# Performance work log

Hardware: AMD Instinct MI355X
Metric: run time of the kernel (lower is better)

## Reference

```python
import jax, jax.numpy as jnp
import numpy as np

B, L, D = 2, 2048, 2048
NUM_HEADS, NUM_KV_HEADS, HEAD_DIM = 8, 4, 256
GROUPS = NUM_HEADS // NUM_KV_HEADS
ROPE_BASE, ROPE_SCALE, ROPE_PROP = 10000.0, 1.0, 1.0
WINDOW = 1024
SOFT_CAP = 50.0
K_MASK = -2.3819763e+38
EPS = 1e-6


def rms_norm(x, scale):
    # RMSNorm(head_dim, with_scale=True, scale_plus_one=False), fp32 internals
    xf = x.astype(jnp.float32)
    var = jnp.mean(jnp.square(xf), axis=-1, keepdims=True)
    return (xf * jax.lax.rsqrt(var + EPS) * scale).astype(x.dtype)


def apply_rope(x, positions):
    # x: [B, L, N, H]; Gemma-style half-split rotation over rope_proportion of H
    H = x.shape[-1]
    rope_dim = int(H * ROPE_PROP)
    half = rope_dim // 2
    freq = ROPE_BASE ** (2.0 * jnp.arange(half, dtype=jnp.float32) / rope_dim)
    t = positions.astype(jnp.float32)[:, :, None] / freq[None, None, :]  # [B,L,half]
    t = t / ROPE_SCALE
    sin = jnp.sin(t)[:, :, None, :]  # [B,L,1,half]
    cos = jnp.cos(t)[:, :, None, :]
    x1 = x[..., :half]
    x2 = x[..., half:rope_dim]
    rotated = jnp.concatenate([x1 * cos - x2 * sin, x2 * cos + x1 * sin], axis=-1)
    if rope_dim < H:
        rotated = jnp.concatenate([rotated, x[..., rope_dim:]], axis=-1)
    return rotated.astype(x.dtype)


def setup_inputs() -> dict:
    key = jax.random.key(0)
    ks = jax.random.split(key, 8)
    x = jax.random.normal(ks[0], (B, L, D), dtype=jnp.float32)
    positions = jnp.broadcast_to(jnp.arange(L, dtype=jnp.int32)[None, :], (B, L))
    attn_mask = jnp.broadcast_to(jnp.tril(jnp.ones((L, L), dtype=bool))[None], (B, L, L))
    s = 0.02
    wq = jax.random.normal(ks[1], (D, NUM_HEADS * HEAD_DIM), dtype=jnp.float32) * s
    wk = jax.random.normal(ks[2], (D, NUM_KV_HEADS * HEAD_DIM), dtype=jnp.float32) * s
    wv = jax.random.normal(ks[3], (D, NUM_KV_HEADS * HEAD_DIM), dtype=jnp.float32) * s
    wo = jax.random.normal(ks[4], (NUM_HEADS * HEAD_DIM, D), dtype=jnp.float32) * s
    q_scale = 1.0 + 0.02 * jax.random.normal(ks[5], (HEAD_DIM,), dtype=jnp.float32)
    k_scale = 1.0 + 0.02 * jax.random.normal(ks[6], (HEAD_DIM,), dtype=jnp.float32)
    return {"x": x, "positions": positions, "attn_mask": attn_mask,
            "wq": wq, "wk": wk, "wv": wv, "wo": wo,
            "q_scale": q_scale, "k_scale": k_scale}


def reference(x, positions, attn_mask, wq, wk, wv, wo, q_scale, k_scale):
    q = (x @ wq).reshape(B, L, NUM_HEADS, HEAD_DIM)
    k = (x @ wk).reshape(B, L, NUM_KV_HEADS, HEAD_DIM)
    v = (x @ wv).reshape(B, L, NUM_KV_HEADS, HEAD_DIM)
    q = rms_norm(q, q_scale)
    k = rms_norm(k, k_scale)
    q = apply_rope(q, positions)
    k = apply_rope(k, positions)
    # query_pre_attn_scalar == 1.0 in source (no-op)
    qg = q.reshape(B, L, NUM_KV_HEADS, GROUPS, HEAD_DIM)
    logits = jnp.einsum('blkgh,bskh->blkgs', qg, k).reshape(B, L, NUM_HEADS, L)
    logits = jnp.tanh(logits / SOFT_CAP) * SOFT_CAP
    # sliding-window mask (LOCAL_SLIDING, no cache -> cache_positions = positions)
    cp = positions[:, None, :]
    pp = positions[:, :, None]
    slide = (cp > pp - WINDOW) & (cp < pp + WINDOW)
    mask = attn_mask & slide  # [B, L, S]
    padded = jnp.where(mask[:, :, None, :], logits, K_MASK)
    probs = jax.nn.softmax(padded, axis=-1).astype(k.dtype)
    pg = probs.reshape(B, L, NUM_KV_HEADS, GROUPS, L)
    out = jnp.einsum('blkgs,bskh->blkgh', pg, v).reshape(B, L, NUM_HEADS * HEAD_DIM)
    return out @ wo
```

## Files before the change

kernel.cpp:

```cpp
#include <hip/hip_runtime.h>
#include <stdint.h>

typedef unsigned short u16;
typedef __bf16 bf16x8 __attribute__((ext_vector_type(8)));
typedef float f32x4 __attribute__((ext_vector_type(4)));

#define SEQ 2048
#define NH 8
#define NKVH 4
#define HD 256
#define WIN 1024
#define NBATCH 2

__device__ __forceinline__ u16 f2bf(float f) {
    union { float f; unsigned u; } v; v.f = f;
    unsigned r = v.u + 0x7FFFu + ((v.u >> 16) & 1u);
    return (u16)(r >> 16);
}
__device__ __forceinline__ float bf2f(u16 h) {
    union { unsigned u; float f; } v; v.u = ((unsigned)h) << 16;
    return v.f;
}
__device__ __forceinline__ bf16x8 ld8(const u16* p) {
    return *reinterpret_cast<const bf16x8*>(p);
}
__device__ __forceinline__ void split2(float f, u16& h, u16& l) {
    h = f2bf(f);
    l = f2bf(f - bf2f(h));
}
__device__ __forceinline__ void gld16(const u16* gp, u16* lp) {
    __builtin_amdgcn_global_load_lds(
        (__attribute__((address_space(1))) unsigned int*)gp,
        (__attribute__((address_space(3))) unsigned int*)lp, 16, 0, 0);
}
#define MFMA16(a, b, c) __builtin_amdgcn_mfma_f32_16x16x32_bf16((a), (b), (c), 0, 0, 0)

__global__ void k_cvt_x(const float* __restrict__ in, u16* __restrict__ hi,
                        u16* __restrict__ lo, int n) {
    int i = (blockIdx.x * blockDim.x + threadIdx.x) * 4;
    if (i >= n) return;
    float4 v = *reinterpret_cast<const float4*>(in + i);
    ushort4 oh, ol;
    split2(v.x, oh.x, ol.x); split2(v.y, oh.y, ol.y);
    split2(v.z, oh.z, ol.z); split2(v.w, oh.w, ol.w);
    *reinterpret_cast<ushort4*>(hi + i) = oh;
    *reinterpret_cast<ushort4*>(lo + i) = ol;
}

__global__ void k_wt(const float* __restrict__ src, u16* __restrict__ dh,
                     u16* __restrict__ dl, int ncols) {
    __shared__ float tile[64][65];
    int c0 = blockIdx.x * 64;
    int k0 = blockIdx.y * 64;
    int tx = threadIdx.x & 63, ty = threadIdx.x >> 6;
    #pragma unroll
    for (int r = 0; r < 16; ++r) {
        int k = k0 + ty * 16 + r;
        tile[ty * 16 + r][tx] = src[(size_t)k * ncols + c0 + tx];
    }
    __syncthreads();
    #pragma unroll
    for (int r = 0; r < 16; ++r) {
        int c = c0 + ty * 16 + r;
        float f = tile[tx][ty * 16 + r];
        u16 h, l; split2(f, h, l);
        dh[(size_t)c * 2048 + k0 + tx] = h;
        dl[(size_t)c * 2048 + k0 + tx] = l;
    }
}

__global__ __launch_bounds__(256, 4) void k_gemm(
        const u16* __restrict__ A0, const u16* __restrict__ B0,
        const u16* __restrict__ A1, const u16* __restrict__ B1,
        const u16* __restrict__ A2, const u16* __restrict__ B2,
        float* __restrict__ C, int M, int N, int K, int nseg, int vcol0) {
    __shared__ __align__(16) u16 sA[128 * 64];
    __shared__ __align__(16) u16 sB[128 * 64];
    const int tm = blockIdx.x * 128;
    const int tn = blockIdx.y * 128;
    const int tid = threadIdx.x;
    const int lane = tid & 63;
    const int wave = tid >> 6;
    const int wr = (wave >> 1) * 64;
    const int wc = (wave & 1) * 64;
    const int l16 = lane & 15;
    const int g = lane >> 4;
    const int srow = tid >> 3;
    const int schunk = tid & 7;
    const int nseg_eff = (tn >= vcol0) ? 1 : nseg;
    f32x4 acc[4][4] = {};

    for (int seg = 0; seg < nseg_eff; ++seg) {
        const u16* A = seg == 0 ? A0 : (seg == 1 ? A1 : A2);
        const u16* B = seg == 0 ? B0 : (seg == 1 ? B1 : B2);
        for (int k0 = 0; k0 < K; k0 += 64) {
            __syncthreads();
            #pragma unroll
            for (int i = 0; i < 4; ++i) {
                int row = i * 32 + srow;
                int cs = ((schunk ^ (row & 7)) << 3);
                gld16(A + (size_t)(tm + row) * K + k0 + cs, &sA[i * 2048 + tid * 8]);
                gld16(B + (size_t)(tn + row) * K + k0 + cs, &sB[i * 2048 + tid * 8]);
            }
            __syncthreads();
            #pragma unroll
            for (int kk = 0; kk < 2; ++kk) {
                const int j = kk * 4 + g;
                bf16x8 af[4], bfv[4];
                #pragma unroll
                for (int m = 0; m < 4; ++m) {
                    int r = wr + m * 16 + l16;
                    af[m] = ld8(&sA[r * 64 + ((j ^ (r & 7)) << 3)]);
                }
                #pragma unroll
                for (int n = 0; n < 4; ++n) {
                    int r = wc + n * 16 + l16;
                    bfv[n] = ld8(&sB[r * 64 + ((j ^ (r & 7)) << 3)]);
                }
                #pragma unroll
                for (int m = 0; m < 4; ++m)
                    #pragma unroll
                    for (int n = 0; n < 4; ++n)
                        acc[m][n] = MFMA16(af[m], bfv[n], acc[m][n]);
            }
        }
    }
    int rbase = tm + wr + g * 4;
    int cbase = tn + wc + l16;
    #pragma unroll
    for (int m = 0; m < 4; ++m)
        #pragma unroll
        for (int n = 0; n < 4; ++n)
            #pragma unroll
            for (int r = 0; r < 4; ++r)
                C[(size_t)(rbase + m * 16 + r) * N + cbase + n * 16] = acc[m][n][r];
}

__global__ __launch_bounds__(256, 3) void k_gemm1(
        const u16* __restrict__ Ah, const u16* __restrict__ Al,
        const u16* __restrict__ Bh, const u16* __restrict__ Bl,
        float* __restrict__ C, int M, int N, int K, int vcol0) {
    __shared__ __align__(16) u16 sAh[128 * 64];
    __shared__ __align__(16) u16 sAl[128 * 64];
    __shared__ __align__(16) u16 sB[128 * 64];
    const int tm = blockIdx.x * 128;
    const int tn = blockIdx.y * 128;
    const int tid = threadIdx.x;
    const int lane = tid & 63;
    const int wave = tid >> 6;
    const int wr = (wave >> 1) * 64;
    const int wc = (wave & 1) * 64;
    const int l16 = lane & 15;
    const int g = lane >> 4;
    const int srow = tid >> 3;
    const int schunk = tid & 7;
    const bool qk = (tn < vcol0);
    f32x4 acc[4][4] = {};

    for (int k0 = 0; k0 < K; k0 += 64) {
        __syncthreads();
        #pragma unroll
        for (int i = 0; i < 4; ++i) {
            int row = i * 32 + srow;
            int cs = ((schunk ^ (row & 7)) << 3);
            gld16(Ah + (size_t)(tm + row) * K + k0 + cs, &sAh[i * 2048 + tid * 8]);
            if (qk)
                gld16(Al + (size_t)(tm + row) * K + k0 + cs, &sAl[i * 2048 + tid * 8]);
            gld16(Bh + (size_t)(tn + row) * K + k0 + cs, &sB[i * 2048 + tid * 8]);
        }
        __syncthreads();
        #pragma unroll
        for (int kk = 0; kk < 2; ++kk) {
            const int j = kk * 4 + g;
            bf16x8 bfv[4], af[4];
            #pragma unroll
            for (int n = 0; n < 4; ++n) {
                int r = wc + n * 16 + l16;
                bfv[n] = ld8(&sB[r * 64 + ((j ^ (r & 7)) << 3)]);
            }
            #pragma unroll
            for (int m = 0; m < 4; ++m) {
                int r = wr + m * 16 + l16;
                af[m] = ld8(&sAh[r * 64 + ((j ^ (r & 7)) << 3)]);
            }
            #pragma unroll
            for (int m = 0; m < 4; ++m)
                #pragma unroll
                for (int n = 0; n < 4; ++n)
                    acc[m][n] = MFMA16(af[m], bfv[n], acc[m][n]);
            if (qk) {
                bf16x8 afl[4];
                #pragma unroll
                for (int m = 0; m < 4; ++m) {
                    int r = wr + m * 16 + l16;
                    afl[m] = ld8(&sAl[r * 64 + ((j ^ (r & 7)) << 3)]);
                }
                #pragma unroll
                for (int m = 0; m < 4; ++m)
                    #pragma unroll
                    for (int n = 0; n < 4; ++n)
                        acc[m][n] = MFMA16(afl[m], bfv[n], acc[m][n]);
            }
        }
    }

    if (qk) {
        for (int k0 = 0; k0 < K; k0 += 64) {
            __syncthreads();
            #pragma unroll
            for (int i = 0; i < 4; ++i) {
                int row = i * 32 + srow;
                int cs = ((schunk ^ (row & 7)) << 3);
                gld16(Ah + (size_t)(tm + row) * K + k0 + cs, &sAh[i * 2048 + tid * 8]);
                gld16(Bl + (size_t)(tn + row) * K + k0 + cs, &sB[i * 2048 + tid * 8]);
            }
            __syncthreads();
            #pragma unroll
            for (int kk = 0; kk < 2; ++kk) {
                const int j = kk * 4 + g;
                bf16x8 bfv[4], af[4];
                #pragma unroll
                for (int n = 0; n < 4; ++n) {
                    int r = wc + n * 16 + l16;
                    bfv[n] = ld8(&sB[r * 64 + ((j ^ (r & 7)) << 3)]);
                }
                #pragma unroll
                for (int m = 0; m < 4; ++m) {
                    int r = wr + m * 16 + l16;
                    af[m] = ld8(&sAh[r * 64 + ((j ^ (r & 7)) << 3)]);
                }
                #pragma unroll
                for (int m = 0; m < 4; ++m)
                    #pragma unroll
                    for (int n = 0; n < 4; ++n)
                        acc[m][n] = MFMA16(af[m], bfv[n], acc[m][n]);
            }
        }
    }

    int rbase = tm + wr + g * 4;
    int cbase = tn + wc + l16;
    #pragma unroll
    for (int m = 0; m < 4; ++m)
        #pragma unroll
        for (int n = 0; n < 4; ++n)
            #pragma unroll
            for (int r = 0; r < 4; ++r)
                C[(size_t)(rbase + m * 16 + r) * N + cbase + n * 16] = acc[m][n][r];
}

__global__ void k_normrope(const float* __restrict__ qkv, const int* __restrict__ pos,
                           const float* __restrict__ qscale, const float* __restrict__ kscale,
                           u16* __restrict__ Qh, u16* __restrict__ Ql,
                           u16* __restrict__ Kh, u16* __restrict__ Kl) {
    int wid = blockIdx.x * 4 + (threadIdx.x >> 6);
    int lane = threadIdx.x & 63;
    const int nq = NBATCH * SEQ * NH;
    const int ntot = NBATCH * SEQ * (NH + NKVH);
    if (wid >= ntot) return;
    const float* scale;
    const float* src;
    u16 *dh, *dl;
    int bt, isq;
    if (wid < nq) {
        int h = wid % NH; bt = wid / NH; isq = 1;
        scale = qscale;
        src = qkv + (size_t)bt * 4096 + h * 256;
        int b = bt >> 11, t = bt & 2047;
        size_t off = (((size_t)b * NH + h) * SEQ + t) * 256;
        dh = Qh + off; dl = Ql + off;
    } else {
        int w2 = wid - nq;
        int h = w2 % NKVH; bt = w2 / NKVH; isq = 0;
        scale = kscale;
        src = qkv + (size_t)bt * 4096 + 2048 + h * 256;
        int b = bt >> 11, t = bt & 2047;
        size_t off = (((size_t)b * NKVH + h) * SEQ + t) * 256;
        dh = Kh + off; dl = Kl + off;
    }
    const int t7 = bt & 7;
    float e[4];
    float ssq = 0.f;
    #pragma unroll
    for (int j = 0; j < 4; ++j) { e[j] = src[lane + 64 * j]; ssq += e[j] * e[j]; }
    #pragma unroll
    for (int off = 1; off < 64; off <<= 1) ssq += __shfl_xor(ssq, off);
    float inv = rsqrtf(ssq * (1.0f / 256.0f) + 1e-6f);
    #pragma unroll
    for (int j = 0; j < 4; ++j) e[j] = e[j] * inv * scale[lane + 64 * j];
    float p = (float)pos[bt];
    float fr0 = powf(10000.0f, (2.0f * lane) * (1.0f / 256.0f));
    float fr1 = powf(10000.0f, (2.0f * (lane + 64)) * (1.0f / 256.0f));
    float s0, c0, s1, c1;
    sincosf(p / fr0, &s0, &c0);
    sincosf(p / fr1, &s1, &c1);
    float rv[4];
    rv[0] = e[0] * c0 - e[2] * s0;
    rv[1] = e[1] * c1 - e[3] * s1;
    rv[2] = e[2] * c0 + e[0] * s0;
    rv[3] = e[3] * c1 + e[1] * s1;
    #pragma unroll
    for (int j = 0; j < 4; ++j) {
        int d = lane + 64 * j;
        int dd = isq ? d : ((((d >> 3) ^ t7) << 3) | (d & 7));
        u16 h, l; split2(rv[j], h, l);
        dh[dd] = h; dl[dd] = l;
    }
}

__global__ void k_vtrans(const float* __restrict__ qkv, u16* __restrict__ VT) {
    __shared__ float tile[64][65];
    int bh = blockIdx.z;
    int d0 = blockIdx.y * 64;
    int t0 = blockIdx.x * 64;
    int b = bh >> 2, h = bh & 3;
    int tx = threadIdx.x & 63, ty = threadIdx.x >> 6;
    #pragma unroll
    for (int r = 0; r < 16; ++r) {
        int t = t0 + ty * 16 + r;
        tile[ty * 16 + r][tx] = qkv[(size_t)(b * SEQ + t) * 4096 + 3072 + h * 256 + d0 + tx];
    }
    __syncthreads();
    #pragma unroll
    for (int r = 0; r < 16; ++r) {
        int d = d0 + ty * 16 + r;
        VT[((size_t)bh * 256 + d) * SEQ + t0 + tx] = f2bf(tile[tx][ty * 16 + r]);
    }
}

__global__ __launch_bounds__(256, 2) void k_attn(const u16* __restrict__ Qh, const u16* __restrict__ Ql,
                                                 const u16* __restrict__ Kh, const u16* __restrict__ Kl,
                                                 const u16* __restrict__ VT,
                                                 u16* __restrict__ Out) {
    __shared__ __align__(16) u16 sKh[32 * 256];
    __shared__ __align__(16) u16 sKl[32 * 256];
    __shared__ __align__(16) u16 sV[256 * 32];
    __shared__ __align__(16) u16 pls[4][16][40];

    const int id = blockIdx.x;
    const int xcd = id & 7;
    const int j = id >> 3;
    const int b  = xcd >> 2;
    const int hk = xcd & 3;
    const int hq = hk * 2 + (j & 1);
    const int qt = 31 - (j >> 1);
    const int tid = threadIdx.x;
    const int lane = tid & 63;
    const int wave = tid >> 6;
    const int q0b = qt * 64;
    const int q0 = q0b + wave * 16;
    const int l16 = lane & 15;
    const int g = lane >> 4;

    bf16x8 qfh[8], qfl[8];
    {
        size_t qoff = (((size_t)b * NH + hq) * SEQ + q0 + l16) * 256 + g * 8;
        #pragma unroll
        for (int kk = 0; kk < 8; ++kk) {
            qfh[kk] = ld8(Qh + qoff + kk * 32);
            qfl[kk] = ld8(Ql + qoff + kk * 32);
        }
    }

    float ssum[4] = {0.f, 0.f, 0.f, 0.f};
    f32x4 o[16] = {};

    const u16* kgh = Kh + (((size_t)b * NKVH + hk) * SEQ) * 256;
    const u16* kgl = Kl + (((size_t)b * NKVH + hk) * SEQ) * 256;
    const u16* vg  = VT + ((size_t)(b * NKVH + hk) * 256) * SEQ;

    int s_lo = q0b - (WIN - 1); if (s_lo < 0) s_lo = 0; s_lo &= ~31;
    const int s_hi = q0b + 63;
    const int ntiles = (s_hi - s_lo) / 32 + 1;

    for (int t = 0; t < ntiles; ++t) {
        const int s0 = s_lo + t * 32;
        __syncthreads();
        {
            const u16* srch = kgh + (size_t)s0 * 256 + tid * 8;
            const u16* srcl = kgl + (size_t)s0 * 256 + tid * 8;
            #pragma unroll
            for (int i = 0; i < 4; ++i) {
                gld16(srch + i * 2048, &sKh[i * 2048 + tid * 8]);
                gld16(srcl + i * 2048, &sKl[i * 2048 + tid * 8]);
            }
            const u16* srcv = vg + (size_t)(tid >> 2) * SEQ + s0 + (tid & 3) * 8;
            #pragma unroll
            for (int i = 0; i < 4; ++i)
                gld16(srcv + (size_t)i * 64 * SEQ, &sV[i * 2048 + tid * 8]);
        }
        __syncthreads();

        if (s0 <= q0 + 15 && s0 + 31 >= q0 - (WIN - 1)) {
            f32x4 c[2] = {};
            __builtin_amdgcn_s_setprio(1);
            #pragma unroll
            for (int kk = 0; kk < 8; ++kk) {
                #pragma unroll
                for (int cc = 0; cc < 2; ++cc) {
                    int row = cc * 16 + l16;
                    int slot = ((kk * 4 + g) ^ (row & 7)) << 3;
                    bf16x8 kh = ld8(&sKh[row * 256 + slot]);
                    bf16x8 kl = ld8(&sKl[row * 256 + slot]);
                    c[cc] = MFMA16(qfh[kk], kh, c[cc]);
                    c[cc] = MFMA16(qfl[kk], kh, c[cc]);
                    c[cc] = MFMA16(qfh[kk], kl, c[cc]);
                }
            }
            __builtin_amdgcn_s_setprio(0);

            const bool full = (s0 + 31 <= q0) && (s0 >= q0 + 15 - (WIN - 1));
            #pragma unroll
            for (int r = 0; r < 4; ++r) {
                int qp = q0 + g * 4 + r;
                int row = g * 4 + r;
                #pragma unroll
                for (int cc = 0; cc < 2; ++cc) {
                    float ev = __expf(c[cc][r] * 0.04f);
                    float v = 50.f - 100.f * __builtin_amdgcn_rcpf(ev + 1.f);
                    if (!full) {
                        int sp = s0 + cc * 16 + l16;
                        bool valid = (sp <= qp) && (sp > qp - WIN);
                        v = valid ? v : -1e30f;
                    }
                    float p = __expf(v - 20.f);
                    u16 pb = f2bf(p);
                    pls[wave][row][cc * 16 + l16] = pb;
                    ssum[r] += bf2f(pb);
                }
            }
            bf16x8 pa = ld8(&pls[wave][l16][g * 8]);
            __builtin_amdgcn_s_setprio(1);
            #pragma unroll
            for (int jb = 0; jb < 16; ++jb)
                o[jb] = MFMA16(pa, ld8(&sV[(jb * 16 + l16) * 32 + g * 8]), o[jb]);
            __builtin_amdgcn_s_setprio(0);
        }
    }

    #pragma unroll
    for (int off = 1; off < 16; off <<= 1)
        #pragma unroll
        for (int r = 0; r < 4; ++r) ssum[r] += __shfl_xor(ssum[r], off);
    #pragma unroll
    for (int r = 0; r < 4; ++r) {
        float inv = 1.0f / ssum[r];
        int trow = q0 + g * 4 + r;
        size_t base = ((size_t)(b * SEQ + trow) * NH + hq) * 256 + l16;
        #pragma unroll
        for (int jb = 0; jb < 16; ++jb)
            Out[base + jb * 16] = f2bf(o[jb][r] * inv);
    }
}

extern "C" void kernel_launch(void* const* d_in, const int* in_sizes, int n_in,
                              void* d_out, int out_size, void* d_ws, size_t ws_size,
                              hipStream_t stream) {
    (void)in_sizes; (void)n_in; (void)out_size; (void)ws_size;
    const float* x  = (const float*)d_in[0];
    const int* pos  = (const int*)d_in[1];
    const float* wq = (const float*)d_in[3];
    const float* wk = (const float*)d_in[4];
    const float* wv = (const float*)d_in[5];
    const float* wo = (const float*)d_in[6];
    const float* qs = (const float*)d_in[7];
    const float* ks = (const float*)d_in[8];

    const size_t MX = (size_t)4096 * 2048;
    const size_t MW = (size_t)2048 * 2048;

    u16* xh  = (u16*)d_ws;
    u16* xl  = xh + MX;
    u16* wth = xl + MX;
    u16* wtl = wth + MX;
    u16* woth = wtl + MX;
    u16* wotl = woth + MW;
    float* qkv = (float*)(wotl + MW);

    u16* qbh = xh;
    u16* qbl = qbh + MX;
    u16* kbh = qbl + MX;
    u16* kbl = kbh + MX / 2;
    u16* vt  = kbl + MX / 2;
    u16* ao  = (u16*)qkv;

    k_cvt_x<<<8192, 256, 0, stream>>>(x, xh, xl, 4096 * 2048);
    k_wt<<<dim3(32, 32), 256, 0, stream>>>(wq, wth, wtl, 2048);
    k_wt<<<dim3(16, 32), 256, 0, stream>>>(wk, wth + MW, wtl + MW, 1024);
    k_wt<<<dim3(16, 32), 256, 0, stream>>>(wv, wth + MW + MW / 2, wtl + MW + MW / 2, 1024);
    k_wt<<<dim3(32, 32), 256, 0, stream>>>(wo, woth, wotl, 2048);
    k_gemm1<<<dim3(32, 32), 256, 0, stream>>>(xh, xl, wth, wtl, qkv,
                                              4096, 4096, 2048, 3072);
    k_normrope<<<12288, 256, 0, stream>>>(qkv, pos, qs, ks, qbh, qbl, kbh, kbl);
    k_vtrans<<<dim3(32, 4, 8), 256, 0, stream>>>(qkv, vt);
    k_attn<<<512, 256, 0, stream>>>(qbh, qbl, kbh, kbl, vt, ao);
    k_gemm<<<dim3(32, 16), 256, 0, stream>>>(ao, woth, ao, woth, ao, wotl, (float*)d_out,
                                             4096, 2048, 2048, 1, 2048);
}
```

Before: 371.2 us.

## Fuse split-bf16 B-low pass into main GEMM K-loop for QK columns

The QKV projection GEMM uses a three-term split-bf16 product (Ah*Bh + Al*Bh + Ah*Bl) for the Q/K columns. Previously the Ah*Bl term ran as a second full K-loop that re-streamed Ah from global memory. Now Bl is staged into its own shared buffer in the same loop, and all three MFMA groups reuse one Ah tile load, removing the redundant Ah traffic and the extra loop overhead. This adds 16KB of LDS per block, so launch bounds drop from 3 to 2 blocks per CU, which may reduce occupancy and latency hiding.

```diff
diff --git a/kernel.cpp b/kernel.cpp
--- a/kernel.cpp
+++ b/kernel.cpp
@@ -136,13 +136,14 @@
                 C[(size_t)(rbase + m * 16 + r) * N + cbase + n * 16] = acc[m][n][r];
 }
 
-__global__ __launch_bounds__(256, 3) void k_gemm1(
+__global__ __launch_bounds__(256, 2) void k_gemm1(
         const u16* __restrict__ Ah, const u16* __restrict__ Al,
         const u16* __restrict__ Bh, const u16* __restrict__ Bl,
         float* __restrict__ C, int M, int N, int K, int vcol0) {
     __shared__ __align__(16) u16 sAh[128 * 64];
     __shared__ __align__(16) u16 sAl[128 * 64];
-    __shared__ __align__(16) u16 sB[128 * 64];
+    __shared__ __align__(16) u16 sBh[128 * 64];
+    __shared__ __align__(16) u16 sBl[128 * 64];
     const int tm = blockIdx.x * 128;
     const int tn = blockIdx.y * 128;
     const int tid = threadIdx.x;
@@ -164,30 +165,32 @@
             int row = i * 32 + srow;
             int cs = ((schunk ^ (row & 7)) << 3);
             gld16(Ah + (size_t)(tm + row) * K + k0 + cs, &sAh[i * 2048 + tid * 8]);
-            if (qk)
+            gld16(Bh + (size_t)(tn + row) * K + k0 + cs, &sBh[i * 2048 + tid * 8]);
+            if (qk) {
                 gld16(Al + (size_t)(tm + row) * K + k0 + cs, &sAl[i * 2048 + tid * 8]);
-            gld16(Bh + (size_t)(tn + row) * K + k0 + cs, &sB[i * 2048 + tid * 8]);
+                gld16(Bl + (size_t)(tn + row) * K + k0 + cs, &sBl[i * 2048 + tid * 8]);
+            }
         }
         __syncthreads();
         #pragma unroll
         for (int kk = 0; kk < 2; ++kk) {
             const int j = kk * 4 + g;
-            bf16x8 bfv[4], af[4];
+            bf16x8 afh[4], bfh[4];
+            #pragma unroll
+            for (int m = 0; m < 4; ++m) {
+                int r = wr + m * 16 + l16;
+                afh[m] = ld8(&sAh[r * 64 + ((j ^ (r & 7)) << 3)]);
+            }
             #pragma unroll
             for (int n = 0; n < 4; ++n) {
                 int r = wc + n * 16 + l16;
-                bfv[n] = ld8(&sB[r * 64 + ((j ^ (r & 7)) << 3)]);
-            }
-            #pragma unroll
-            for (int m = 0; m < 4; ++m) {
-                int r = wr + m * 16 + l16;
-                af[m] = ld8(&sAh[r * 64 + ((j ^ (r & 7)) << 3)]);
+                bfh[n] = ld8(&sBh[r * 64 + ((j ^ (r & 7)) << 3)]);
             }
             #pragma unroll
             for (int m = 0; m < 4; ++m)
                 #pragma unroll
                 for (int n = 0; n < 4; ++n)
-                    acc[m][n] = MFMA16(af[m], bfv[n], acc[m][n]);
+                    acc[m][n] = MFMA16(afh[m], bfh[n], acc[m][n]);
             if (qk) {
                 bf16x8 afl[4];
                 #pragma unroll
@@ -199,41 +202,18 @@
                 for (int m = 0; m < 4; ++m)
                     #pragma unroll
                     for (int n = 0; n < 4; ++n)
-                        acc[m][n] = MFMA16(afl[m], bfv[n], acc[m][n]);
-            }
-        }
-    }
-
-    if (qk) {
-        for (int k0 = 0; k0 < K; k0 += 64) {
-            __syncthreads();
-            #pragma unroll
-            for (int i = 0; i < 4; ++i) {
-                int row = i * 32 + srow;
-                int cs = ((schunk ^ (row & 7)) << 3);
-                gld16(Ah + (size_t)(tm + row) * K + k0 + cs, &sAh[i * 2048 + tid * 8]);
-                gld16(Bl + (size_t)(tn + row) * K + k0 + cs, &sB[i * 2048 + tid * 8]);
-            }
-            __syncthreads();
-            #pragma unroll
-            for (int kk = 0; kk < 2; ++kk) {
-                const int j = kk * 4 + g;
-                bf16x8 bfv[4], af[4];
+                        acc[m][n] = MFMA16(afl[m], bfh[n], acc[m][n]);
+                bf16x8 bfl[4];
                 #pragma unroll
                 for (int n = 0; n < 4; ++n) {
                     int r = wc + n * 16 + l16;
-                    bfv[n] = ld8(&sB[r * 64 + ((j ^ (r & 7)) << 3)]);
-                }
-                #pragma unroll
-                for (int m = 0; m < 4; ++m) {
-                    int r = wr + m * 16 + l16;
-                    af[m] = ld8(&sAh[r * 64 + ((j ^ (r & 7)) << 3)]);
+                    bfl[n] = ld8(&sBl[r * 64 + ((j ^ (r & 7)) << 3)]);
                 }
                 #pragma unroll
                 for (int m = 0; m < 4; ++m)
                     #pragma unroll
                     for (int n = 0; n < 4; ++n)
-                        acc[m][n] = MFMA16(af[m], bfv[n], acc[m][n]);
+                        acc[m][n] = MFMA16(afh[m], bfl[n], acc[m][n]);
             }
         }
     }
```

Result: no change. 370.7 us (-0.1%).
